# Kernel optimization log

Measured on AMD Instinct MI355X. Metric: run time of the kernel, lower is better.

The kernel has to match this reference:

```python
import jax, jax.numpy as jnp
import numpy as np

D_MODEL = 2048
N_HEAD = 16
HEAD_DIM = D_MODEL // N_HEAD
D_FF = 8192
SEQ = 2048
PAST = 2048
BATCH = 2
LN_EPS = 1e-5


def setup_inputs() -> dict:
    key = jax.random.key(0)
    ks = jax.random.split(key, 16)
    s = 0.02  # weight init scale
    return {
        "x": jax.random.normal(ks[0], (SEQ, BATCH, D_MODEL), jnp.float32),
        "k_cache": jax.random.normal(ks[1], (PAST, BATCH, N_HEAD, HEAD_DIM), jnp.float32),
        "v_cache": jax.random.normal(ks[2], (PAST, BATCH, N_HEAD, HEAD_DIM), jnp.float32),
        "mask": jnp.zeros((SEQ, PAST + SEQ), jnp.float32),
        "q_w": jax.random.normal(ks[3], (D_MODEL, D_MODEL), jnp.float32) * s,
        "q_b": jnp.zeros((D_MODEL,), jnp.float32),
        "k_w": jax.random.normal(ks[4], (D_MODEL, D_MODEL), jnp.float32) * s,
        "k_b": jnp.zeros((D_MODEL,), jnp.float32),
        "v_w": jax.random.normal(ks[5], (D_MODEL, D_MODEL), jnp.float32) * s,
        "v_b": jnp.zeros((D_MODEL,), jnp.float32),
        "o_w": jax.random.normal(ks[6], (D_MODEL, D_MODEL), jnp.float32) * s,
        "o_b": jnp.zeros((D_MODEL,), jnp.float32),
        "ln1_g": jnp.ones((D_MODEL,), jnp.float32),
        "ln1_b": jnp.zeros((D_MODEL,), jnp.float32),
        "ln2_g": jnp.ones((D_MODEL,), jnp.float32),
        "ln2_b": jnp.zeros((D_MODEL,), jnp.float32),
        "w1": jax.random.normal(ks[7], (D_MODEL, D_FF), jnp.float32) * s,
        "b1": jnp.zeros((D_FF,), jnp.float32),
        "w2": jax.random.normal(ks[8], (D_FF, D_MODEL), jnp.float32) * s,
        "b2": jnp.zeros((D_MODEL,), jnp.float32),
    }


def _layernorm(y, g, b):
    m = jnp.mean(y, axis=-1, keepdims=True)
    v = jnp.var(y, axis=-1, keepdims=True)  # biased var, matches torch LayerNorm
    return (y - m) * jax.lax.rsqrt(v + LN_EPS) * g + b


def reference(x, k_cache, v_cache, mask, q_w, q_b, k_w, k_b, v_w, v_b, o_w, o_b,
              ln1_g, ln1_b, ln2_g, ln2_b, w1, b1, w2, b2):
    S, B, D = x.shape
    H, hd = N_HEAD, HEAD_DIM

    x_norm = _layernorm(x, ln1_g, ln1_b)
    q = (x_norm @ q_w + q_b).reshape(S, B, H, hd)
    k = (x_norm @ k_w + k_b).reshape(S, B, H, hd)
    v = (x_norm @ v_w + v_b).reshape(S, B, H, hd)

    k_full = jnp.concatenate([k_cache, k], axis=0)  # [T,B,H,hd], T = past+S
    v_full = jnp.concatenate([v_cache, v], axis=0)

    # scores: [B,H,S,T]
    scores = jnp.einsum('sbhd,tbhd->bhst', q, k_full) / (hd ** 0.5)
    scores = scores + mask  # mask [S,T] broadcasts over B,H
    attn = jax.nn.softmax(scores, axis=-1)
    out = jnp.einsum('bhst,tbhd->sbhd', attn, v_full).reshape(S, B, D)
    x = x + out @ o_w + o_b

    h = _layernorm(x, ln2_g, ln2_b)
    x = x + jax.nn.gelu(h @ w1 + b1, approximate=False) @ w2 + b2
    return (x, k_full, v_full)
```

## Files before the change

kernel.cpp:

```cpp
#include <hip/hip_runtime.h>
#include <hip/hip_bf16.h>


typedef __bf16 bf16x8 __attribute__((ext_vector_type(8)));
typedef float f32x4 __attribute__((ext_vector_type(4)));
typedef float f32x16 __attribute__((ext_vector_type(16)));
typedef unsigned int u32;

__device__ __forceinline__ unsigned short f2bf(float f) {
  union { float f; unsigned u; } v; v.f = f;
  return (unsigned short)((v.u + 0x7FFFu + ((v.u >> 16) & 1u)) >> 16);
}

__device__ __forceinline__ float fexp2(float x) {
#if __has_builtin(__builtin_amdgcn_exp2f)
  return __builtin_amdgcn_exp2f(x);
#else
  float r;
  asm volatile("v_exp_f32 %0, %1\ns_nop 0" : "=v"(r) : "v"(x));
  return r;
#endif
}

__device__ __forceinline__ void gl16(const void* g, void* l) {
  __builtin_amdgcn_global_load_lds((__attribute__((address_space(1))) void*)g,
                                   (__attribute__((address_space(3))) void*)l,
                                   16, 0, 0);
}

__global__ __launch_bounds__(256) void ln_k(const float* __restrict__ X,
                                            const float* __restrict__ G,
                                            const float* __restrict__ Bb,
                                            unsigned short* __restrict__ Y) {
  const int row = blockIdx.x;
  const int tid = threadIdx.x;
  const float4* xr = (const float4*)(X + (size_t)row * 2048);
  const float4 xa = xr[tid], xb = xr[tid + 256];
  float s = xa.x + xa.y + xa.z + xa.w + xb.x + xb.y + xb.z + xb.w;
  float q = xa.x * xa.x + xa.y * xa.y + xa.z * xa.z + xa.w * xa.w +
            xb.x * xb.x + xb.y * xb.y + xb.z * xb.z + xb.w * xb.w;
  for (int off = 32; off; off >>= 1) {
    s += __shfl_xor(s, off);
    q += __shfl_xor(q, off);
  }
  __shared__ float red[8];
  const int wv = tid >> 6, ln = tid & 63;
  if (ln == 0) { red[wv] = s; red[4 + wv] = q; }
  __syncthreads();
  s = red[0] + red[1] + red[2] + red[3];
  q = red[4] + red[5] + red[6] + red[7];
  const float mean = s * (1.f / 2048.f);
  const float rstd = rsqrtf(q * (1.f / 2048.f) - mean * mean + 1e-5f);
  const float4 g0 = ((const float4*)G)[tid], g1 = ((const float4*)G)[tid + 256];
  const float4 b0 = ((const float4*)Bb)[tid], b1 = ((const float4*)Bb)[tid + 256];
  ushort4 o0, o1;
  o0.x = f2bf((xa.x - mean) * rstd * g0.x + b0.x);
  o0.y = f2bf((xa.y - mean) * rstd * g0.y + b0.y);
  o0.z = f2bf((xa.z - mean) * rstd * g0.z + b0.z);
  o0.w = f2bf((xa.w - mean) * rstd * g0.w + b0.w);
  o1.x = f2bf((xb.x - mean) * rstd * g1.x + b1.x);
  o1.y = f2bf((xb.y - mean) * rstd * g1.y + b1.y);
  o1.z = f2bf((xb.z - mean) * rstd * g1.z + b1.z);
  o1.w = f2bf((xb.w - mean) * rstd * g1.w + b1.w);
  ((ushort4*)(Y + (size_t)row * 2048))[tid] = o0;
  ((ushort4*)(Y + (size_t)row * 2048))[tid + 256] = o1;
}

__global__ __launch_bounds__(256) void wconvT(const float* __restrict__ W,
                                              unsigned short* __restrict__ Wt,
                                              int K, int N) {
  __shared__ float tl[32][33];
  const int k0 = blockIdx.x * 32, n0 = blockIdx.y * 32;
  const int x = threadIdx.x & 31, y = threadIdx.x >> 5;
  for (int i = 0; i < 4; ++i)
    tl[y + i * 8][x] = W[(size_t)(k0 + y + i * 8) * N + n0 + x];
  __syncthreads();
  for (int i = 0; i < 4; ++i)
    Wt[(size_t)(n0 + y + i * 8) * K + k0 + x] = f2bf(tl[x][y + i * 8]);
}

__global__ __launch_bounds__(256) void wconvT4(const float* __restrict__ Wq,
                                               const float* __restrict__ Wk,
                                               const float* __restrict__ Wv,
                                               const float* __restrict__ Wo,
                                               unsigned short* __restrict__ Wt) {
  __shared__ float tl[32][33];
  const int z = blockIdx.z;
  const float* W = z == 0 ? Wq : (z == 1 ? Wk : (z == 2 ? Wv : Wo));
  unsigned short* dst = Wt + (size_t)z * 2048 * 2048;
  const int k0 = blockIdx.x * 32, n0 = blockIdx.y * 32;
  const int x = threadIdx.x & 31, y = threadIdx.x >> 5;
  for (int i = 0; i < 4; ++i)
    tl[y + i * 8][x] = W[(size_t)(k0 + y + i * 8) * 2048 + n0 + x];
  __syncthreads();
  for (int i = 0; i < 4; ++i)
    dst[(size_t)(n0 + y + i * 8) * 2048 + k0 + x] = f2bf(tl[x][y + i * 8]);
}

__global__ __launch_bounds__(256) void kpack(const float* __restrict__ src,
                                             unsigned short* __restrict__ dstb,
                                             float* __restrict__ dstf) {
  const size_t e = ((size_t)blockIdx.x * 256 + threadIdx.x) * 4;
  const int r = (int)(e >> 11), c = (int)(e & 2047);
  const int t = r >> 1, b = r & 1, h = c >> 7, d = c & 127;
  const float4 v = *(const float4*)(src + e);
  ushort4 o;
  o.x = f2bf(v.x); o.y = f2bf(v.y); o.z = f2bf(v.z); o.w = f2bf(v.w);
  *(ushort4*)(dstb + ((size_t)((b * 16 + h) * 4096 + t)) * 128 + d) = o;
  *(float4*)(dstf + (size_t)r * 2048 + c) = v;
}

__global__ __launch_bounds__(256) void vtrans(const float* __restrict__ src,
                                              unsigned short* __restrict__ dstb,
                                              float* __restrict__ dstf) {
  __shared__ float tl[32][33];
  const int bh = blockIdx.z;
  const int b = bh >> 4, h = bh & 15;
  const int t0 = blockIdx.x * 32, d0 = blockIdx.y * 32;
  const int x = threadIdx.x & 31, y = threadIdx.x >> 5;
  for (int i = 0; i < 4; ++i) {
    const int t = t0 + y + i * 8, d = d0 + x;
    const float v = src[((size_t)(t * 2 + b) * 16 + h) * 128 + d];
    tl[y + i * 8][x] = v;
    dstf[((size_t)(t * 2 + b) * 16 + h) * 128 + d] = v;
  }
  __syncthreads();
  for (int i = 0; i < 4; ++i) {
    const int d = d0 + y + i * 8, t = t0 + x;
    dstb[((size_t)bh * 128 + d) * 4096 + t] = f2bf(tl[x][y + i * 8]);
  }
}

__global__ __launch_bounds__(256) void mask0_k(const float* __restrict__ mask,
                                               u32* __restrict__ flags) {
  const float4* p = (const float4*)mask + (size_t)blockIdx.x * 8192 + threadIdx.x;
  int nz = 0;
#pragma unroll
  for (int i = 0; i < 32; ++i) {
    const float4 v = p[i * 256];
    nz |= (v.x != 0.f) | (v.y != 0.f) | (v.z != 0.f) | (v.w != 0.f);
  }
  const int r = __syncthreads_or(nz);
  if (threadIdx.x == 0) flags[blockIdx.x] = (u32)r;
}

template <int TAG, int EPI>
__global__ __launch_bounds__(512, 2) void gemm8p(
    const unsigned short* __restrict__ A, const unsigned short* __restrict__ Bt,
    const float* __restrict__ bias, const float* __restrict__ bias2,
    const float* __restrict__ bias3,
    float* __restrict__ Cf, unsigned short* __restrict__ Cb,
    float* __restrict__ of2, unsigned short* __restrict__ pb2,
    unsigned short* __restrict__ pb3, int N, int K) {
  __shared__ unsigned short sA[2][256 * 64];
  __shared__ unsigned short sB[2][256 * 64];
  const int tid = threadIdx.x;
  const int wv = tid >> 6, ln = tid & 63;
  const int wm = wv >> 2, wn = wv & 3;
  const int nwg = gridDim.x;
  const int bid = blockIdx.x;
  const int wk = (bid & 7) * (nwg >> 3) + (bid >> 3);
  const int nmt = 16;
  const int m0 = (wk & (nmt - 1)) * 256, n0 = (wk / nmt) * 256;
  const int NT = K >> 6, NI = NT >> 1;

  f32x4 acc[8][4] = {};
  bf16x8 af[4][2], bfr[2][2];

  auto ST = [&](int t, int which, int bb) {
    if (t >= NT) return;
    const unsigned short* G = (which < 2) ? A : Bt;
    const int base0 = ((which < 2) ? m0 : n0) + (which & 1) * 128;
    char* dst = (char*)((which < 2) ? &sA[bb][0] : &sB[bb][0]) + (which & 1) * 16384;
    const size_t kb = (size_t)t * 64;
#pragma unroll
    for (int c = 0; c < 2; ++c) {
      const int o = tid * 16 + c * 8192;
      const int row = o >> 7;
      const int cb = (o & 127) ^ ((row & 7) << 4);
      gl16((const char*)G + ((size_t)(base0 + row) * K + kb) * 2 + cb, dst + o);
    }
  };
  auto LDA = [&](int bb, int mh) {
    const char* base = (const char*)&sA[bb][0];
#pragma unroll
    for (int i = 0; i < 4; ++i) {
      const int r = wm * 128 + mh * 64 + i * 16 + (ln & 15);
#pragma unroll
      for (int kk = 0; kk < 2; ++kk) {
        int aa = (r << 7) + ((ln >> 4) << 4) + kk * 64;
        aa ^= (r & 7) << 4;
        af[i][kk] = *(const bf16x8*)(base + aa);
      }
    }
  };
  auto LDB = [&](int bb, int nh) {
    const char* base = (const char*)&sB[bb][0];
#pragma unroll
    for (int j = 0; j < 2; ++j) {
      const int r = wn * 64 + nh * 32 + j * 16 + (ln & 15);
#pragma unroll
      for (int kk = 0; kk < 2; ++kk) {
        int aa = (r << 7) + ((ln >> 4) << 4) + kk * 64;
        aa ^= (r & 7) << 4;
        bfr[j][kk] = *(const bf16x8*)(base + aa);
      }
    }
  };
  auto MM = [&](int mh, int nh) {
    __builtin_amdgcn_s_setprio(1);
#pragma unroll
    for (int i = 0; i < 4; ++i)
#pragma unroll
      for (int j = 0; j < 2; ++j)
#pragma unroll
        for (int kk = 0; kk < 2; ++kk)
          acc[mh * 4 + i][nh * 2 + j] = __builtin_amdgcn_mfma_f32_16x16x32_bf16(
              af[i][kk], bfr[j][kk], acc[mh * 4 + i][nh * 2 + j], 0, 0, 0);
    __builtin_amdgcn_s_setprio(0);
  };
#define BAR() __builtin_amdgcn_s_barrier()
#define VM2() asm volatile("s_waitcnt vmcnt(2)" ::: "memory")
#define VM0() asm volatile("s_waitcnt vmcnt(0)" ::: "memory")

  ST(0, 0, 0); ST(0, 1, 0); ST(0, 2, 0); ST(0, 3, 0); ST(1, 0, 1);
  VM2();
  BAR();

#pragma unroll 1
  for (int it = 0; it < NI; ++it) {
    const int t1 = 2 * it + 1, t2 = 2 * it + 2, t3 = 2 * it + 3;
    const bool lastit = (it == NI - 1);
    LDA(0, 0); LDB(0, 0); ST(t1, 1, 1); BAR(); MM(0, 0); BAR();
    LDB(0, 1);            ST(t1, 2, 1); BAR(); MM(0, 1); BAR();
    LDA(0, 1);            ST(t1, 3, 1); BAR(); MM(1, 1); BAR();
    LDB(0, 0);            ST(t2, 0, 0); BAR(); MM(1, 0);
    if (lastit) VM0(); else VM2();
    BAR();
    LDA(1, 0); LDB(1, 0); ST(t2, 1, 0); BAR(); MM(0, 0); BAR();
    LDB(1, 1);            ST(t2, 2, 0); BAR(); MM(0, 1); BAR();
    LDA(1, 1);            ST(t2, 3, 0); BAR(); MM(1, 1); BAR();
    LDB(1, 0);            ST(t3, 0, 1); BAR(); MM(1, 0);
    if (!lastit) VM2();
    BAR();
  }
#undef BAR
#undef VM2
#undef VM0

  const int lr = (ln >> 4) << 2, lc = ln & 15;
  if (EPI == 0) {
    const int seg = n0 >> 11;
    const float* bp = seg == 0 ? bias : (seg == 1 ? bias2 : bias3);
#pragma unroll
    for (int f = 0; f < 8; ++f) {
#pragma unroll
      for (int j = 0; j < 4; ++j) {
        const int nn = (n0 & 2047) + wn * 64 + j * 16 + lc;
        const int h = nn >> 7, d = nn & 127;
        const float bv = bp[nn];
#pragma unroll
        for (int r = 0; r < 4; ++r) {
          const int m = m0 + wm * 128 + f * 16 + lr + r;
          const int s = m >> 1, b = m & 1;
          const float v = acc[f][j][r] + bv;
          if (seg == 0) {
            Cb[((size_t)(b * 16 + h) * 2048 + s) * 128 + d] = f2bf(v);
          } else if (seg == 1) {
            pb2[((size_t)(b * 16 + h) * 4096 + 2048 + s) * 128 + d] = f2bf(v);
            Cf[((size_t)((2048 + s) * 2 + b) * 16 + h) * 128 + d] = v;
          } else {
            pb3[((size_t)(b * 16 + h) * 128 + d) * 4096 + 2048 + s] = f2bf(v);
            of2[((size_t)((2048 + s) * 2 + b) * 16 + h) * 128 + d] = v;
          }
        }
      }
    }
  } else {
#pragma unroll
    for (int f = 0; f < 8; ++f) {
#pragma unroll
      for (int j = 0; j < 4; ++j) {
        const int n = n0 + wn * 64 + j * 16 + lc;
        const float bv = bias[n];
#pragma unroll
        for (int r = 0; r < 4; ++r) {
          const int m = m0 + wm * 128 + f * 16 + lr + r;
          float v = acc[f][j][r] + bv;
          v = 0.5f * v * (1.f + erff(v * 0.7071067811865476f));
          Cb[(size_t)m * N + n] = f2bf(v);
        }
      }
    }
  }
}

template <int TAG, int EPI>
__global__ __launch_bounds__(512, 2) void gemm8n(
    const unsigned short* __restrict__ A, const unsigned short* __restrict__ Bt,
    const float* __restrict__ bias, const float* __restrict__ Rsd,
    float* __restrict__ Cf, int N, int K) {
  __shared__ unsigned short sA[2][128 * 64];
  __shared__ unsigned short sB[2][256 * 64];
  const int tid = threadIdx.x;
  const int wv = tid >> 6, ln = tid & 63;
  const int wm = wv >> 2, wn = wv & 3;
  const int nwg = gridDim.x;
  const int bid = blockIdx.x;
  const int wk = (bid & 7) * (nwg >> 3) + (bid >> 3);
  const int m0 = (wk & 31) * 128, n0 = (wk >> 5) * 256;
  const int NT = K >> 6;

  f32x4 acc[4][4] = {};
  bf16x8 af[2][2], bfr[2][2];

  auto ST = [&](int t, int which, int bb) {
    if (t >= NT) return;
    const unsigned short* G = (which == 0) ? A : Bt;
    const int base0 = (which == 0) ? m0 : (which == 1 ? n0 : n0 + 128);
    char* dst = (which == 0) ? (char*)&sA[bb][0]
                             : (char*)&sB[bb][0] + (which - 1) * 16384;
    const size_t kb = (size_t)t * 64;
#pragma unroll
    for (int c = 0; c < 2; ++c) {
      const int o = tid * 16 + c * 8192;
      const int row = o >> 7;
      const int cb = (o & 127) ^ ((row & 7) << 4);
      gl16((const char*)G + ((size_t)(base0 + row) * K + kb) * 2 + cb, dst + o);
    }
  };
  auto LDA = [&](int bb, int mh) {
    const char* base = (const char*)&sA[bb][0];
#pragma unroll
    for (int i = 0; i < 2; ++i) {
      const int r = wm * 64 + mh * 32 + i * 16 + (ln & 15);
#pragma unroll
      for (int kk = 0; kk < 2; ++kk) {
        int aa = (r << 7) + ((ln >> 4) << 4) + kk * 64;
        aa ^= (r & 7) << 4;
        af[i][kk] = *(const bf16x8*)(base + aa);
      }
    }
  };
  auto LDB = [&](int bb, int nh) {
    const char* base = (const char*)&sB[bb][0];
#pragma unroll
    for (int j = 0; j < 2; ++j) {
      const int r = wn * 64 + nh * 32 + j * 16 + (ln & 15);
#pragma unroll
      for (int kk = 0; kk < 2; ++kk) {
        int aa = (r << 7) + ((ln >> 4) << 4) + kk * 64;
        aa ^= (r & 7) << 4;
        bfr[j][kk] = *(const bf16x8*)(base + aa);
      }
    }
  };
  auto MM = [&](int mh, int nh) {
    __builtin_amdgcn_s_setprio(1);
#pragma unroll
    for (int i = 0; i < 2; ++i)
#pragma unroll
      for (int j = 0; j < 2; ++j)
#pragma unroll
        for (int kk = 0; kk < 2; ++kk)
          acc[mh * 2 + i][nh * 2 + j] = __builtin_amdgcn_mfma_f32_16x16x32_bf16(
              af[i][kk], bfr[j][kk], acc[mh * 2 + i][nh * 2 + j], 0, 0, 0);
    __builtin_amdgcn_s_setprio(0);
  };
#define BAR() __builtin_amdgcn_s_barrier()
#define VM2() asm volatile("s_waitcnt vmcnt(2)" ::: "memory")
#define VM0() asm volatile("s_waitcnt vmcnt(0)" ::: "memory")

  ST(0, 0, 0); ST(0, 1, 0); ST(0, 2, 0); ST(1, 0, 1);
  VM2();
  BAR();

#pragma unroll 1
  for (int t = 0; t < NT; ++t) {
    const int cur = t & 1;
    LDA(cur, 0); LDB(cur, 0); ST(t + 1, 1, cur ^ 1); BAR(); MM(0, 0); BAR();
    LDB(cur, 1); ST(t + 1, 2, cur ^ 1); BAR(); MM(0, 1); BAR();
    LDA(cur, 1); BAR(); MM(1, 1); BAR();
    LDB(cur, 0); ST(t + 2, 0, cur); BAR(); MM(1, 0);
    if (t >= NT - 2) VM0(); else VM2();
    BAR();
  }
#undef BAR
#undef VM2
#undef VM0

  const int lr = (ln >> 4) << 2, lc = ln & 15;
#pragma unroll
  for (int i = 0; i < 4; ++i) {
#pragma unroll
    for (int j = 0; j < 4; ++j) {
      const int n = n0 + wn * 64 + j * 16 + lc;
      const float bv = bias[n];
#pragma unroll
      for (int r = 0; r < 4; ++r) {
        const int m = m0 + wm * 64 + i * 16 + lr + r;
        const float v = acc[i][j][r] + bv + Rsd[(size_t)m * N + n];
        Cf[(size_t)m * N + n] = v;
      }
    }
  }
}

__global__ __launch_bounds__(256, 2) void attn6(
    const unsigned short* __restrict__ Q,
    const unsigned short* __restrict__ Kf,
    const unsigned short* __restrict__ Vt,
    const float* __restrict__ mask,
    const u32* __restrict__ flags,
    unsigned short* __restrict__ ctx) {
  __shared__ __attribute__((aligned(16))) char smem[65536];
  const int tid = threadIdx.x;
  const int wv = tid >> 6;
  const int ln = tid & 63;
  const int q = ln & 31;
  const int hi = ln >> 5;
  const int sw = (q & 7) << 4;
  const int bh = blockIdx.y;
  const int s0w = blockIdx.x * 128 + wv * 32;

  const int mnz = __syncthreads_or((int)flags[tid]);

  bf16x8 qreg[8];
  {
    const char* qsrc = (const char*)Q +
        ((size_t)bh * 2048 + s0w + q) * 256 + (hi << 4);
#pragma unroll
    for (int kk = 0; kk < 8; ++kk) qreg[kk] = *(const bf16x8*)(qsrc + kk * 32);
  }

  const char* kp[8];
  const char* vp[4];
#pragma unroll
  for (int kk = 0; kk < 8; ++kk)
    kp[kk] = smem + (q << 8) + (((kk << 5) + (hi << 4)) ^ sw);
#pragma unroll
  for (int kk = 0; kk < 4; ++kk)
    vp[kk] = smem + 32768 + (q << 7) + (((kk << 5) + (hi << 4)) ^ sw);

  const char* Kg;
  const char* Vg;
  {
    const int oo = tid * 16;
    const int kr = oo >> 8, kc = oo & 255;
    Kg = (const char*)Kf + (size_t)bh * 4096 * 256 + (size_t)kr * 256 +
         (kc ^ ((kr & 7) << 4));
    const int vr = oo >> 7, vc = oo & 127;
    Vg = (const char*)Vt + (size_t)bh * 128 * 8192 + (size_t)vr * 8192 +
         (vc ^ ((vr & 7) << 4));
  }
  char* kdst = smem + tid * 16;
  char* vdst = smem + 32768 + tid * 16;

#define STG(BUF)                                               \
  do {                                                         \
    _Pragma("unroll") for (int is = 0; is < 4; ++is) {         \
      gl16(Kg + is * 4096, kdst + (BUF) + is * 4096);          \
      gl16(Vg + (size_t)is * 262144, vdst + (BUF) + is * 4096);\
    }                                                          \
    Kg += 16384; Vg += 128;                                    \
  } while (0)
#define BARR() __builtin_amdgcn_s_barrier()
#define VMW8() asm volatile("s_waitcnt vmcnt(8)" ::: "memory")
#define VMW0() asm volatile("s_waitcnt vmcnt(0)" ::: "memory")

  f32x16 acc[4] = {};
  float m = -1e30f, l = 0.f;
  const float KLOG = 0.127517445f;

  auto tile = [&](int BUF, int it) {
    f32x16 sc0, sc1;
    {
      f32x16 za = {}, zb = {}, zc = {}, zd = {};
      __builtin_amdgcn_s_setprio(1);
#pragma unroll
      for (int kk = 0; kk < 4; ++kk) {
        za = __builtin_amdgcn_mfma_f32_32x32x16_bf16(
            *(const bf16x8*)(kp[kk] + BUF), qreg[kk], za, 0, 0, 0);
        zb = __builtin_amdgcn_mfma_f32_32x32x16_bf16(
            *(const bf16x8*)(kp[kk + 4] + BUF), qreg[kk + 4], zb, 0, 0, 0);
        zc = __builtin_amdgcn_mfma_f32_32x32x16_bf16(
            *(const bf16x8*)(kp[kk] + BUF + 8192), qreg[kk], zc, 0, 0, 0);
        zd = __builtin_amdgcn_mfma_f32_32x32x16_bf16(
            *(const bf16x8*)(kp[kk + 4] + BUF + 8192), qreg[kk + 4], zd, 0, 0, 0);
      }
      __builtin_amdgcn_s_setprio(0);
      sc0 = za + zb;
      sc1 = zc + zd;
    }

    if (mnz) {
      const float rs = 11.313708498984761f;
#pragma unroll
      for (int r = 0; r < 16; ++r) {
        const int tt = it * 64 + ((r & 3) + ((r >> 2) << 3) + (hi << 2));
        sc0[r] = fmaf(mask[(size_t)(s0w + q) * 4096 + tt], rs, sc0[r]);
        sc1[r] = fmaf(mask[(size_t)(s0w + q) * 4096 + tt + 32], rs, sc1[r]);
      }
    }

    float pmax = sc0[0];
#pragma unroll
    for (int r = 1; r < 16; ++r) pmax = fmaxf(pmax, sc0[r]);
#pragma unroll
    for (int r = 0; r < 16; ++r) pmax = fmaxf(pmax, sc1[r]);
    pmax = fmaxf(pmax, __shfl_xor(pmax, 32));
    if (__any(pmax > m + 90.5f)) {
      const float mn = fmaxf(m, pmax);
      const float corr = fexp2((m - mn) * KLOG);
      m = mn; l *= corr;
#pragma unroll
      for (int d4 = 0; d4 < 4; ++d4)
#pragma unroll
        for (int e = 0; e < 16; ++e) acc[d4][e] *= corr;
    }
    const float mk = m * KLOG;
    float rsum = 0.f;
#pragma unroll
    for (int r = 0; r < 16; ++r) {
      const float e = fexp2(fmaf(sc0[r], KLOG, -mk));
      sc0[r] = e;
      rsum += e;
    }
#pragma unroll
    for (int r = 0; r < 16; ++r) {
      const float e = fexp2(fmaf(sc1[r], KLOG, -mk));
      sc1[r] = e;
      rsum += e;
    }
    rsum += __shfl_xor(rsum, 32);
    l += rsum;

    bf16x8 pw[4];
#pragma unroll
    for (int kk = 0; kk < 4; ++kk) {
      const int rb = (kk & 1) * 8;
      u32 w0, w1, w2, w3;
      if (kk < 2) {
        asm("v_cvt_pk_bf16_f32 %0, %1, %2" : "=v"(w0) : "v"(sc0[rb + 0]), "v"(sc0[rb + 1]));
        asm("v_cvt_pk_bf16_f32 %0, %1, %2" : "=v"(w1) : "v"(sc0[rb + 2]), "v"(sc0[rb + 3]));
        asm("v_cvt_pk_bf16_f32 %0, %1, %2" : "=v"(w2) : "v"(sc0[rb + 4]), "v"(sc0[rb + 5]));
        asm("v_cvt_pk_bf16_f32 %0, %1, %2" : "=v"(w3) : "v"(sc0[rb + 6]), "v"(sc0[rb + 7]));
      } else {
        asm("v_cvt_pk_bf16_f32 %0, %1, %2" : "=v"(w0) : "v"(sc1[rb + 0]), "v"(sc1[rb + 1]));
        asm("v_cvt_pk_bf16_f32 %0, %1, %2" : "=v"(w1) : "v"(sc1[rb + 2]), "v"(sc1[rb + 3]));
        asm("v_cvt_pk_bf16_f32 %0, %1, %2" : "=v"(w2) : "v"(sc1[rb + 4]), "v"(sc1[rb + 5]));
        asm("v_cvt_pk_bf16_f32 %0, %1, %2" : "=v"(w3) : "v"(sc1[rb + 6]), "v"(sc1[rb + 7]));
      }
      asm("v_permlane32_swap_b32 %0, %1" : "+v"(w0), "+v"(w2));
      asm("v_permlane32_swap_b32 %0, %1" : "+v"(w1), "+v"(w3));
      union { u32 u[4]; bf16x8 b; } pk;
      pk.u[0] = w0; pk.u[1] = w1; pk.u[2] = w2; pk.u[3] = w3;
      pw[kk] = pk.b;
    }

#pragma unroll
    for (int d4 = 0; d4 < 4; ++d4) {
      __builtin_amdgcn_s_setprio(1);
#pragma unroll
      for (int kk = 0; kk < 4; ++kk)
        acc[d4] = __builtin_amdgcn_mfma_f32_32x32x16_bf16(
            *(const bf16x8*)(vp[kk] + BUF + d4 * 4096), pw[kk], acc[d4], 0, 0, 0);
      __builtin_amdgcn_s_setprio(0);
    }
  };

  STG(0);
  STG(16384);
#pragma unroll 1
  for (int it2 = 0; it2 < 31; ++it2) {
    VMW8(); BARR();
    tile(0, 2 * it2);
    BARR();
    STG(0);
    VMW8(); BARR();
    tile(16384, 2 * it2 + 1);
    BARR();
    STG(16384);
  }
  VMW8(); BARR();
  tile(0, 62);
  BARR();
  VMW0(); BARR();
  tile(16384, 63);
#undef STG
#undef BARR
#undef VMW8
#undef VMW0

  const float inv = 1.f / l;
  const int b = bh >> 4, h = bh & 15;
  unsigned short* crow = ctx + ((size_t)(s0w + q) * 2 + b) * 2048 + h * 128;
#pragma unroll
  for (int d4 = 0; d4 < 4; ++d4)
#pragma unroll
    for (int r = 0; r < 16; ++r) {
      const int d = d4 * 32 + (r & 3) + ((r >> 2) << 3) + (hi << 2);
      crow[d] = f2bf(acc[d4][r] * inv);
    }
}

extern "C" void kernel_launch(void* const* d_in, const int* in_sizes, int n_in,
                              void* d_out, int out_size, void* d_ws, size_t ws_size,
                              hipStream_t stream) {
  const float* x    = (const float*)d_in[0];
  const float* kc   = (const float*)d_in[1];
  const float* vc   = (const float*)d_in[2];
  const float* mask = (const float*)d_in[3];
  const float* q_w  = (const float*)d_in[4];
  const float* q_b  = (const float*)d_in[5];
  const float* k_w  = (const float*)d_in[6];
  const float* k_b  = (const float*)d_in[7];
  const float* v_w  = (const float*)d_in[8];
  const float* v_b  = (const float*)d_in[9];
  const float* o_w  = (const float*)d_in[10];
  const float* o_b  = (const float*)d_in[11];
  const float* ln1g = (const float*)d_in[12];
  const float* ln1b = (const float*)d_in[13];
  const float* ln2g = (const float*)d_in[14];
  const float* ln2b = (const float*)d_in[15];
  const float* w1   = (const float*)d_in[16];
  const float* b1   = (const float*)d_in[17];
  const float* w2   = (const float*)d_in[18];
  const float* b2   = (const float*)d_in[19];

  float* out_x = (float*)d_out;
  float* out_k = out_x + (size_t)8388608;
  float* out_v = out_k + (size_t)16777216;

  char* ws = (char*)d_ws;
  unsigned short* kf  = (unsigned short*)(ws);
  unsigned short* vft = (unsigned short*)(ws + 33554432);
  unsigned short* Wt  = (unsigned short*)(ws + 67108864);
  float*          x1  = (float*)(ws + 100663296);
  unsigned short* mid = (unsigned short*)ws;
  u32* mflags = (u32*)(ws + 100663296);

  unsigned short* xn  = (unsigned short*)d_out;
  unsigned short* ctx = xn;
  unsigned short* qb  = (unsigned short*)((char*)d_out + 16777216);
  unsigned short* hn  = qb;

  const dim3 b256(256);

  ln_k<<<4096, b256, 0, stream>>>(x, ln1g, ln1b, xn);
  kpack<<<8192, b256, 0, stream>>>(kc, kf, out_k);
  vtrans<<<dim3(64, 4, 32), b256, 0, stream>>>(vc, vft, out_v);
  mask0_k<<<256, b256, 0, stream>>>(mask, mflags);

  wconvT4<<<dim3(64, 64, 4), b256, 0, stream>>>(q_w, k_w, v_w, o_w, Wt);

  gemm8p<0, 0><<<384, dim3(512), 0, stream>>>(
      xn, Wt, q_b, k_b, v_b, out_k, qb, out_v, kf, vft, 6144, 2048);

  attn6<<<dim3(16, 32), b256, 0, stream>>>(qb, kf, vft, mask, mflags, ctx);

  gemm8n<1, 1><<<256, dim3(512), 0, stream>>>(
      ctx, Wt + (size_t)6144 * 2048, o_b, x, x1, 2048, 2048);

  ln_k<<<4096, b256, 0, stream>>>(x1, ln2g, ln2b, hn);

  wconvT<<<dim3(64, 256), b256, 0, stream>>>(w1, Wt, 2048, 8192);
  gemm8p<2, 2><<<512, dim3(512), 0, stream>>>(
      hn, Wt, b1, nullptr, nullptr, nullptr, mid, nullptr, nullptr, nullptr,
      8192, 2048);

  wconvT<<<dim3(256, 64), b256, 0, stream>>>(w2, Wt, 8192, 2048);
  gemm8n<3, 1><<<256, dim3(512), 0, stream>>>(
      mid, Wt, b2, x1, out_x, 2048, 8192);
}
```

Before: 885.1 us.

## Use 128x256 double-buffered GEMM with single barrier pair for QKV and N-GEMMs

Replaces gemm8n with a new gemm2b kernel that prefetches two full K-tiles ahead, waits with vmcnt(6), and runs all four A fragments per step with two barriers per iteration instead of eight. The QKV projection now uses this 128x256 tile kernel with 768 blocks instead of the 256x256 gemm8p with 384, which gives more blocks at the cost of a smaller tile. gemm8p is reduced to the GELU epilogue only. The intent is to cut barrier overhead and improve load/compute overlap, with more register pressure from holding more A fragments.

```diff
diff --git a/kernel.cpp b/kernel.cpp
--- a/kernel.cpp
+++ b/kernel.cpp
@@ -147,11 +147,8 @@
 template <int TAG, int EPI>
 __global__ __launch_bounds__(512, 2) void gemm8p(
     const unsigned short* __restrict__ A, const unsigned short* __restrict__ Bt,
-    const float* __restrict__ bias, const float* __restrict__ bias2,
-    const float* __restrict__ bias3,
-    float* __restrict__ Cf, unsigned short* __restrict__ Cb,
-    float* __restrict__ of2, unsigned short* __restrict__ pb2,
-    unsigned short* __restrict__ pb3, int N, int K) {
+    const float* __restrict__ bias, unsigned short* __restrict__ Cb,
+    int N, int K) {
   __shared__ unsigned short sA[2][256 * 64];
   __shared__ unsigned short sB[2][256 * 64];
   const int tid = threadIdx.x;
@@ -249,11 +246,127 @@
 #undef VM0
 
   const int lr = (ln >> 4) << 2, lc = ln & 15;
+#pragma unroll
+  for (int f = 0; f < 8; ++f) {
+#pragma unroll
+    for (int j = 0; j < 4; ++j) {
+      const int n = n0 + wn * 64 + j * 16 + lc;
+      const float bv = bias[n];
+#pragma unroll
+      for (int r = 0; r < 4; ++r) {
+        const int m = m0 + wm * 128 + f * 16 + lr + r;
+        float v = acc[f][j][r] + bv;
+        v = 0.5f * v * (1.f + erff(v * 0.7071067811865476f));
+        Cb[(size_t)m * N + n] = f2bf(v);
+      }
+    }
+  }
+}
+
+template <int TAG, int EPI>
+__global__ __launch_bounds__(512, 2) void gemm2b(
+    const unsigned short* __restrict__ A, const unsigned short* __restrict__ Bt,
+    const float* __restrict__ bias, const float* __restrict__ bias2,
+    const float* __restrict__ bias3, const float* __restrict__ Rsd,
+    float* __restrict__ Cf, unsigned short* __restrict__ Cb,
+    float* __restrict__ of2, unsigned short* __restrict__ pb2,
+    unsigned short* __restrict__ pb3, int N, int K) {
+  __shared__ unsigned short sA[2][128 * 64];
+  __shared__ unsigned short sB[2][256 * 64];
+  const int tid = threadIdx.x;
+  const int wv = tid >> 6, ln = tid & 63;
+  const int wm = wv >> 2, wn = wv & 3;
+  const int nwg = gridDim.x;
+  const int bid = blockIdx.x;
+  const int wk = (bid & 7) * (nwg >> 3) + (bid >> 3);
+  const int m0 = (wk & 31) * 128, n0 = (wk >> 5) * 256;
+  const int NT = K >> 6;
+
+  f32x4 acc[4][4] = {};
+  bf16x8 af[4][2], bfr[2][2];
+
+  auto ST = [&](int t, int which, int bb) {
+    if (t >= NT) return;
+    const unsigned short* G = (which == 0) ? A : Bt;
+    const int base0 = (which == 0) ? m0 : (which == 1 ? n0 : n0 + 128);
+    char* dst = (which == 0) ? (char*)&sA[bb][0]
+                             : (char*)&sB[bb][0] + (which - 1) * 16384;
+    const size_t kb = (size_t)t * 64;
+#pragma unroll
+    for (int c = 0; c < 2; ++c) {
+      const int o = tid * 16 + c * 8192;
+      const int row = o >> 7;
+      const int cb = (o & 127) ^ ((row & 7) << 4);
+      gl16((const char*)G + ((size_t)(base0 + row) * K + kb) * 2 + cb, dst + o);
+    }
+  };
+  auto LDA = [&](int bb) {
+    const char* base = (const char*)&sA[bb][0];
+#pragma unroll
+    for (int i = 0; i < 4; ++i) {
+      const int r = wm * 64 + i * 16 + (ln & 15);
+#pragma unroll
+      for (int kk = 0; kk < 2; ++kk) {
+        int aa = (r << 7) + ((ln >> 4) << 4) + kk * 64;
+        aa ^= (r & 7) << 4;
+        af[i][kk] = *(const bf16x8*)(base + aa);
+      }
+    }
+  };
+  auto LDB = [&](int bb, int nh) {
+    const char* base = (const char*)&sB[bb][0];
+#pragma unroll
+    for (int j = 0; j < 2; ++j) {
+      const int r = wn * 64 + nh * 32 + j * 16 + (ln & 15);
+#pragma unroll
+      for (int kk = 0; kk < 2; ++kk) {
+        int aa = (r << 7) + ((ln >> 4) << 4) + kk * 64;
+        aa ^= (r & 7) << 4;
+        bfr[j][kk] = *(const bf16x8*)(base + aa);
+      }
+    }
+  };
+  auto MM = [&](int nh) {
+    __builtin_amdgcn_s_setprio(1);
+#pragma unroll
+    for (int i = 0; i < 4; ++i)
+#pragma unroll
+      for (int j = 0; j < 2; ++j)
+#pragma unroll
+        for (int kk = 0; kk < 2; ++kk)
+          acc[i][nh * 2 + j] = __builtin_amdgcn_mfma_f32_16x16x32_bf16(
+              af[i][kk], bfr[j][kk], acc[i][nh * 2 + j], 0, 0, 0);
+    __builtin_amdgcn_s_setprio(0);
+  };
+#define BARR() __builtin_amdgcn_s_barrier()
+#define VMW6() asm volatile("s_waitcnt vmcnt(6)" ::: "memory")
+#define VMW0() asm volatile("s_waitcnt vmcnt(0)" ::: "memory")
+
+  ST(0, 0, 0); ST(0, 1, 0); ST(0, 2, 0);
+  ST(1, 0, 1); ST(1, 1, 1); ST(1, 2, 1);
+
+#pragma unroll 1
+  for (int t = 0; t < NT; ++t) {
+    const int cur = t & 1;
+    if (t + 1 < NT) VMW6(); else VMW0();
+    BARR();
+    LDA(cur); LDB(cur, 0);
+    MM(0);
+    LDB(cur, 1);
+    MM(1);
+    BARR();
+    ST(t + 2, 0, cur); ST(t + 2, 1, cur); ST(t + 2, 2, cur);
+  }
+#undef BARR
+#undef VMW6
+#undef VMW0
+
+  const int lr = (ln >> 4) << 2, lc = ln & 15;
   if (EPI == 0) {
     const int seg = n0 >> 11;
     const float* bp = seg == 0 ? bias : (seg == 1 ? bias2 : bias3);
 #pragma unroll
-    for (int f = 0; f < 8; ++f) {
+    for (int i = 0; i < 4; ++i) {
 #pragma unroll
       for (int j = 0; j < 4; ++j) {
         const int nn = (n0 & 2047) + wn * 64 + j * 16 + lc;
@@ -261,9 +374,9 @@
         const float bv = bp[nn];
 #pragma unroll
         for (int r = 0; r < 4; ++r) {
-          const int m = m0 + wm * 128 + f * 16 + lr + r;
+          const int m = m0 + wm * 64 + i * 16 + lr + r;
           const int s = m >> 1, b = m & 1;
-          const float v = acc[f][j][r] + bv;
+          const float v = acc[i][j][r] + bv;
           if (seg == 0) {
             Cb[((size_t)(b * 16 + h) * 2048 + s) * 128 + d] = f2bf(v);
           } else if (seg == 1) {
@@ -278,129 +391,17 @@
     }
   } else {
 #pragma unroll
-    for (int f = 0; f < 8; ++f) {
+    for (int i = 0; i < 4; ++i) {
 #pragma unroll
       for (int j = 0; j < 4; ++j) {
         const int n = n0 + wn * 64 + j * 16 + lc;
         const float bv = bias[n];
 #pragma unroll
         for (int r = 0; r < 4; ++r) {
-          const int m = m0 + wm * 128 + f * 16 + lr + r;
-          float v = acc[f][j][r] + bv;
-          v = 0.5f * v * (1.f + erff(v * 0.7071067811865476f));
-          Cb[(size_t)m * N + n] = f2bf(v);
+          const int m = m0 + wm * 64 + i * 16 + lr + r;
+          const float v = acc[i][j][r] + bv + Rsd[(size_t)m * N + n];
+          Cf[(size_t)m * N + n] = v;
         }
-      }
-    }
-  }
-}
-
-template <int TAG, int EPI>
-__global__ __launch_bounds__(512, 2) void gemm8n(
-    const unsigned short* __restrict__ A, const unsigned short* __restrict__ Bt,
-    const float* __restrict__ bias, const float* __restrict__ Rsd,
-    float* __restrict__ Cf, int N, int K) {
-  __shared__ unsigned short sA[2][128 * 64];
-  __shared__ unsigned short sB[2][256 * 64];
-  const int tid = threadIdx.x;
-  const int wv = tid >> 6, ln = tid & 63;
-  const int wm = wv >> 2, wn = wv & 3;
-  const int nwg = gridDim.x;
-  const int bid = blockIdx.x;
-  const int wk = (bid & 7) * (nwg >> 3) + (bid >> 3);
-  const int m0 = (wk & 31) * 128, n0 = (wk >> 5) * 256;
-  const int NT = K >> 6;
-
-  f32x4 acc[4][4] = {};
-  bf16x8 af[2][2], bfr[2][2];
-
-  auto ST = [&](int t, int which, int bb) {
-    if (t >= NT) return;
-    const unsigned short* G = (which == 0) ? A : Bt;
-    const int base0 = (which == 0) ? m0 : (which == 1 ? n0 : n0 + 128);
-    char* dst = (which == 0) ? (char*)&sA[bb][0]
-                             : (char*)&sB[bb][0] + (which - 1) * 16384;
-    const size_t kb = (size_t)t * 64;
-#pragma unroll
-    for (int c = 0; c < 2; ++c) {
-      const int o = tid * 16 + c * 8192;
-      const int row = o >> 7;
-      const int cb = (o & 127) ^ ((row & 7) << 4);
-      gl16((const char*)G + ((size_t)(base0 + row) * K + kb) * 2 + cb, dst + o);
-    }
-  };
-  auto LDA = [&](int bb, int mh) {
-    const char* base = (const char*)&sA[bb][0];
-#pragma unroll
-    for (int i = 0; i < 2; ++i) {
-      const int r = wm * 64 + mh * 32 + i * 16 + (ln & 15);
-#pragma unroll
-      for (int kk = 0; kk < 2; ++kk) {
-        int aa = (r << 7) + ((ln >> 4) << 4) + kk * 64;
-        aa ^= (r & 7) << 4;
-        af[i][kk] = *(const bf16x8*)(base + aa);
-      }
-    }
-  };
-  auto LDB = [&](int bb, int nh) {
-    const char* base = (const char*)&sB[bb][0];
-#pragma unroll
-    for (int j = 0; j < 2; ++j) {
-      const int r = wn * 64 + nh * 32 + j * 16 + (ln & 15);
-#pragma unroll
-      for (int kk = 0; kk < 2; ++kk) {
-        int aa = (r << 7) + ((ln >> 4) << 4) + kk * 64;
-        aa ^= (r & 7) << 4;
-        bfr[j][kk] = *(const bf16x8*)(base + aa);
-      }
-    }
-  };
-  auto MM = [&](int mh, int nh) {
-    __builtin_amdgcn_s_setprio(1);
-#pragma unroll
-    for (int i = 0; i < 2; ++i)
-#pragma unroll
-      for (int j = 0; j < 2; ++j)
-#pragma unroll
-        for (int kk = 0; kk < 2; ++kk)
-          acc[mh * 2 + i][nh * 2 + j] = __builtin_amdgcn_mfma_f32_16x16x32_bf16(
-              af[i][kk], bfr[j][kk], acc[mh * 2 + i][nh * 2 + j], 0, 0, 0);
-    __builtin_amdgcn_s_setprio(0);
-  };
-#define BAR() __builtin_amdgcn_s_barrier()
-#define VM2() asm volatile("s_waitcnt vmcnt(2)" ::: "memory")
-#define VM0() asm volatile("s_waitcnt vmcnt(0)" ::: "memory")
-
-  ST(0, 0, 0); ST(0, 1, 0); ST(0, 2, 0); ST(1, 0, 1);
-  VM2();
-  BAR();
-
-#pragma unroll 1
-  for (int t = 0; t < NT; ++t) {
-    const int cur = t & 1;
-    LDA(cur, 0); LDB(cur, 0); ST(t + 1, 1, cur ^ 1); BAR(); MM(0, 0); BAR();
-    LDB(cur, 1); ST(t + 1, 2, cur ^ 1); BAR(); MM(0, 1); BAR();
-    LDA(cur, 1); BAR(); MM(1, 1); BAR();
-    LDB(cur, 0); ST(t + 2, 0, cur); BAR(); MM(1, 0);
-    if (t >= NT - 2) VM0(); else VM2();
-    BAR();
-  }
-#undef BAR
-#undef VM2
-#undef VM0
-
-  const int lr = (ln >> 4) << 2, lc = ln & 15;
-#pragma unroll
-  for (int i = 0; i < 4; ++i) {
-#pragma unroll
-    for (int j = 0; j < 4; ++j) {
-      const int n = n0 + wn * 64 + j * 16 + lc;
-      const float bv = bias[n];
-#pragma unroll
-      for (int r = 0; r < 4; ++r) {
-        const int m = m0 + wm * 64 + i * 16 + lr + r;
-        const float v = acc[i][j][r] + bv + Rsd[(size_t)m * N + n];
-        Cf[(size_t)m * N + n] = v;
       }
     }
   }
@@ -654,22 +655,22 @@
 
   wconvT4<<<dim3(64, 64, 4), b256, 0, stream>>>(q_w, k_w, v_w, o_w, Wt);
 
-  gemm8p<0, 0><<<384, dim3(512), 0, stream>>>(
-      xn, Wt, q_b, k_b, v_b, out_k, qb, out_v, kf, vft, 6144, 2048);
+  gemm2b<0, 0><<<768, dim3(512), 0, stream>>>(
+      xn, Wt, q_b, k_b, v_b, nullptr, out_k, qb, out_v, kf, vft, 6144, 2048);
 
   attn6<<<dim3(16, 32), b256, 0, stream>>>(qb, kf, vft, mask, mflags, ctx);
 
-  gemm8n<1, 1><<<256, dim3(512), 0, stream>>>(
-      ctx, Wt + (size_t)6144 * 2048, o_b, x, x1, 2048, 2048);
+  gemm2b<1, 1><<<256, dim3(512), 0, stream>>>(
+      ctx, Wt + (size_t)6144 * 2048, o_b, nullptr, nullptr, x, x1,
+      nullptr, nullptr, nullptr, nullptr, 2048, 2048);
 
   ln_k<<<4096, b256, 0, stream>>>(x1, ln2g, ln2b, hn);
 
   wconvT<<<dim3(64, 256), b256, 0, stream>>>(w1, Wt, 2048, 8192);
-  gemm8p<2, 2><<<512, dim3(512), 0, stream>>>(
-      hn, Wt, b1, nullptr, nullptr, nullptr, mid, nullptr, nullptr, nullptr,
-      8192, 2048);
+  gemm8p<2, 2><<<512, dim3(512), 0, stream>>>(hn, Wt, b1, mid, 8192, 2048);
 
   wconvT<<<dim3(256, 64), b256, 0, stream>>>(w2, Wt, 8192, 2048);
-  gemm8n<3, 1><<<256, dim3(512), 0, stream>>>(
-      mid, Wt, b2, x1, out_x, 2048, 8192);
-}
+  gemm2b<3, 1><<<256, dim3(512), 0, stream>>>(
+      mid, Wt, b2, nullptr, nullptr, x1, out_x, nullptr, nullptr, nullptr, nullptr,
+      2048, 8192);
+}
```

New measurement: 913.2 us. +3.2%, slower.
